# Kernel tuning notes

Hardware: AMD Instinct MI355X
Metric: run time of the kernel (lower is better)

Reference implementation:

```python
import jax, jax.numpy as jnp
import numpy as np

N, E, IN, HID, OUT, B = 50000, 800000, 128, 128, 64, 4096
EPS = 1e-5


def setup_inputs() -> dict:
    key = jax.random.key(0)
    ks = jax.random.split(key, 12)
    x = jax.random.normal(ks[0], (N, IN), jnp.float32)
    edge_index = jax.random.randint(ks[1], (2, E), 0, N, dtype=jnp.int32).astype(jnp.int64)
    target_index = jax.random.randint(ks[2], (B,), 0, N, dtype=jnp.int32).astype(jnp.int64)

    def lin(k, i, o):
        return jax.random.normal(k, (i, o), jnp.float32) * (1.0 / np.sqrt(i))

    return {
        'x': x, 'edge_index': edge_index, 'target_index': target_index,
        'W0': lin(ks[3], IN, HID), 'b0': jnp.zeros((HID,), jnp.float32),
        'W1': lin(ks[4], HID, HID), 'b1': jnp.zeros((HID,), jnp.float32),
        'W2': lin(ks[5], HID, HID), 'b2': jnp.zeros((HID,), jnp.float32),
        'g0': jnp.ones((HID,), jnp.float32), 'bt0': jnp.zeros((HID,), jnp.float32),
        'g1': jnp.ones((HID,), jnp.float32), 'bt1': jnp.zeros((HID,), jnp.float32),
        'f1w': lin(ks[6], HID, HID), 'f1b': jnp.zeros((HID,), jnp.float32),
        'f2w': lin(ks[7], HID, OUT), 'f2b': jnp.zeros((OUT,), jnp.float32),
    }


def _gcn_layer(h, W, b, src, dst, norm):
    # GCNConv: D^-1/2 (A+I) D^-1/2 (h W) + b  (self-loops already in src/dst)
    h = h @ W                                        # [N, out]
    msg = h[src] * norm[:, None]                     # [E+N, out]
    return jax.ops.segment_sum(msg, dst, num_segments=N) + b


def _batchnorm(h, g, bt):
    mu = jnp.mean(h, axis=0)
    var = jnp.mean((h - mu) ** 2, axis=0)            # biased, as torch BN
    return g * (h - mu) * jax.lax.rsqrt(var + EPS) + bt


def reference(x, edge_index, target_index, W0, b0, W1, b1, W2, b2,
              g0, bt0, g1, bt1, f1w, f1b, f2w, f2b):
    loop = jnp.arange(N, dtype=edge_index.dtype)
    src = jnp.concatenate([edge_index[0], loop])
    dst = jnp.concatenate([edge_index[1], loop])
    deg = jax.ops.segment_sum(jnp.ones_like(dst, jnp.float32), dst, num_segments=N)
    dinv = jax.lax.rsqrt(deg)                        # deg >= 1 via self-loops
    norm = dinv[src] * dinv[dst]                     # [E+N]

    h = _gcn_layer(x, W0, b0, src, dst, norm)
    h = jax.nn.relu(_batchnorm(h, g0, bt0))
    h = _gcn_layer(h, W1, b1, src, dst, norm)
    h = jax.nn.relu(_batchnorm(h, g1, bt1))
    h = _gcn_layer(h, W2, b2, src, dst, norm)

    # target_index.unsqueeze(1).expand(-1,-1) -> [B,1]; pool squeezes dim 1
    t = h[target_index]                              # [B, HID]
    t = jax.nn.relu(t @ f1w + f1b)                   # FeedForwardNetwork layer1 (dropout=0)
    return t @ f2w + f2b                             # [B, OUT]
```

## Files before the change

### kernel.cpp

```cpp
#include <hip/hip_runtime.h>


static const int GNN5566_NN  = 50000;
static const int GNN5566_NE  = 800000;
static const int GNN5566_NB  = 4096;
static const int GNN5566_CAP = 64;

static const int GNN5566_NBUCK  = (GNN5566_NN + 63) / 64;
static const int GNN5566_NCHUNK = 64;
static const int GNN5566_CHUNK  = GNN5566_NE / GNN5566_NCHUNK;

static const int GNN5566_WSLOT = 17408;

typedef short gnn5566_s16x8 __attribute__((ext_vector_type(8)));
typedef float gnn5566_f32x4 __attribute__((ext_vector_type(4)));

static __device__ inline float gnn5566_b2f(unsigned short h){
  return __uint_as_float(((unsigned int)h) << 16);
}
static __device__ inline unsigned short gnn5566_f2b(float f){
  unsigned int u = __float_as_uint(f);
  u += 0x7fffu + ((u >> 16) & 1u);
  return (unsigned short)(u >> 16);
}
static __device__ inline float gnn5566_loadf(const void* p, long long i, int isF32){
  if (isF32) return ((const float*)p)[i];
  return gnn5566_b2f(((const unsigned short*)p)[i]);
}

__global__ void GNNEncoder_5566277616090_prep(const void* W0, const void* W1,
                                              const void* W2, const void* f1w,
                                              const void* f2w, unsigned short* wT,
                                              const int* ei, const int* tgt,
                                              int* flags, int* done,
                                              unsigned int* histT){
  __shared__ unsigned short lt[128][129];
  __shared__ int h[GNN5566_NBUCK];
  __shared__ int sFlag;
  int b = blockIdx.x, tid = threadIdx.x;

  if (b == 69) {
    if (tid < 8) done[tid] = 0;
    if (tid < 64) {
      int o1 = ei[2*tid + 1];
      int o2 = tgt[2*tid + 1];
      unsigned int w = ((const unsigned int*)W0)[tid];
      unsigned int e = (w >> 7) & 255u;
      unsigned long long m1 = __ballot(o1 != 0);
      unsigned long long m2 = __ballot(o2 != 0);
      unsigned long long m3 = __ballot(e >= 96u && e <= 134u);
      if (tid == 0) {
        flags[0] = (m1 == 0ull) ? 1 : 0;
        flags[1] = (m2 == 0ull) ? 1 : 0;
        flags[2] = (__popcll(m3) >= 56) ? 0 : 1;
      }
    }
    return;
  }

  if (b >= 64) {
    if (tid < 64) {
      unsigned int w = ((const unsigned int*)W0)[tid];
      unsigned int e = (w >> 7) & 255u;
      unsigned long long m3 = __ballot(e >= 96u && e <= 134u);
      if (tid == 0) sFlag = (__popcll(m3) >= 56) ? 0 : 1;
    }
    __syncthreads();
    int f32 = sFlag;
    int slot = b - 64;
    const void* src = (slot == 0) ? W0 : (slot == 1) ? W1 : (slot == 2) ? W2
                    : (slot == 3) ? f1w : f2w;
    int wide = (slot != 4);
    int tot = wide ? 16384 : 8192;
    for (int i = tid; i < tot; i += 256) {
      int k = wide ? (i >> 7) : (i >> 6);
      int c = wide ? (i & 127) : (i & 63);
      lt[k][c] = f32 ? gnn5566_f2b(((const float*)src)[i])
                     : ((const unsigned short*)src)[i];
    }
    __syncthreads();
    unsigned short* out = wT + slot * GNN5566_WSLOT;
    int wtot = wide ? 2048 : 1024;
    for (int j = tid; j < wtot; j += 256) {
      int c = j >> 4, k8 = (j & 15) << 3;
      unsigned int p0 = (unsigned int)lt[k8    ][c] | ((unsigned int)lt[k8+1][c] << 16);
      unsigned int p1 = (unsigned int)lt[k8 + 2][c] | ((unsigned int)lt[k8+3][c] << 16);
      unsigned int p2 = (unsigned int)lt[k8 + 4][c] | ((unsigned int)lt[k8+5][c] << 16);
      unsigned int p3 = (unsigned int)lt[k8 + 6][c] | ((unsigned int)lt[k8+7][c] << 16);
      uint4 v; v.x = p0; v.y = p1; v.z = p2; v.w = p3;
      *(uint4*)(out + c * 136 + k8) = v;
    }
    return;
  }

  if (tid < 64) {
    int o1 = ei[2*tid + 1];
    unsigned long long m1 = __ballot(o1 != 0);
    if (tid == 0) sFlag = (m1 == 0ull) ? 1 : 0;
  }
  for (int i = tid; i < GNN5566_NBUCK; i += 256) h[i] = 0;
  __syncthreads();
  int f = sFlag;
  int base = b * GNN5566_CHUNK;
  for (int i = tid; i < GNN5566_CHUNK; i += 256) {
    int e = base + i;
    int d = f ? ((const int2*)ei)[GNN5566_NE + e].x : ei[GNN5566_NE + e];
    atomicAdd(&h[d >> 6], 1);
  }
  __syncthreads();
  for (int i = tid; i < GNN5566_NBUCK; i += 256)
    histT[i * GNN5566_NCHUNK + b] = (unsigned int)h[i];
}

__global__ void GNNEncoder_5566277616090_fillS1(unsigned int* histT, int* btot,
                                                int* segStart, int* doneCtr){
  __shared__ int sv[256];
  __shared__ int lastFlag;
  int tid  = threadIdx.x;
  int wv   = (int)(blockIdx.x * 4u + (tid >> 6));
  int lane = tid & 63;

  if (wv < GNN5566_NBUCK) {
    unsigned int* row = histT + wv * GNN5566_NCHUNK;
    int s = (int)row[lane];
    int incl = s;
    #pragma unroll
    for (int off = 1; off < 64; off <<= 1) {
      int t = __shfl_up(incl, off, 64);
      if (lane >= off) incl += t;
    }
    row[lane] = (unsigned int)(incl - s);
    if (lane == 63) atomicExch(&btot[wv], incl);
  }
  __syncthreads();
  if (tid == 0) {
    __threadfence();
    lastFlag = (atomicAdd(doneCtr, 1) == (int)gridDim.x - 1);
  }
  __syncthreads();
  if (!lastFlag) return;

  int i0 = tid * 4;
  int v0 = (i0     < GNN5566_NBUCK) ? atomicAdd(&btot[i0    ], 0) : 0;
  int v1 = (i0 + 1 < GNN5566_NBUCK) ? atomicAdd(&btot[i0 + 1], 0) : 0;
  int v2 = (i0 + 2 < GNN5566_NBUCK) ? atomicAdd(&btot[i0 + 2], 0) : 0;
  int v3 = (i0 + 3 < GNN5566_NBUCK) ? atomicAdd(&btot[i0 + 3], 0) : 0;
  int t01 = v0 + v1, t012 = t01 + v2, T = t012 + v3;
  sv[tid] = T;
  __syncthreads();
  for (int off = 1; off < 256; off <<= 1) {
    int add = (tid >= off) ? sv[tid - off] : 0;
    __syncthreads();
    sv[tid] += add;
    __syncthreads();
  }
  int excl = sv[tid] - T;
  if (i0     < GNN5566_NBUCK) segStart[i0]     = excl;
  if (i0 + 1 < GNN5566_NBUCK) segStart[i0 + 1] = excl + v0;
  if (i0 + 2 < GNN5566_NBUCK) segStart[i0 + 2] = excl + t01;
  if (i0 + 3 < GNN5566_NBUCK) segStart[i0 + 3] = excl + t012;
  if (tid == 0) segStart[GNN5566_NBUCK] = GNN5566_NE;
}

__global__ void GNNEncoder_5566277616090_fillScatter(const int* ei,
                                                     const unsigned int* histT,
                                                     const int* segStart,
                                                     unsigned int* sorted,
                                                     const int* flags){
  __shared__ int cur[GNN5566_NBUCK];
  int tid = threadIdx.x, chunk = blockIdx.x;
  for (int b = tid; b < GNN5566_NBUCK; b += 256)
    cur[b] = (int)histT[b * GNN5566_NCHUNK + chunk] + segStart[b];
  __syncthreads();
  int f = flags[0];
  int base = chunk * GNN5566_CHUNK;
  for (int i = tid; i < GNN5566_CHUNK; i += 256) {
    int e = base + i;
    int s = f ? ((const int2*)ei)[e].x                : ei[e];
    int d = f ? ((const int2*)ei)[GNN5566_NE + e].x   : ei[GNN5566_NE + e];
    int p = atomicAdd(&cur[d >> 6], 1);
    sorted[p] = ((unsigned int)s << 6) | (unsigned int)(d & 63);
  }
}

__global__ void GNNEncoder_5566277616090_fillB(const int* segStart,
                                               const unsigned int* sorted,
                                               unsigned short* colIdx16, int* cnt,
                                               float* dinv){
  __shared__ unsigned int lbuf[64 * 32];
  __shared__ int lcnt[64];
  int b   = blockIdx.x;
  int tid = threadIdx.x;
  if (tid < 64) lcnt[tid] = 0;
  __syncthreads();

  int s0 = segStart[b];
  int n  = segStart[b + 1] - s0;
  const unsigned int* bp = sorted + s0;
  unsigned short* lists = (unsigned short*)lbuf;
  for (int i = tid; i < n; i += 256) {
    unsigned int w = bp[i];
    int d = (int)(w & 63u);
    int s = (int)(w >> 6);
    int p = atomicAdd(&lcnt[d], 1);
    if (p < GNN5566_CAP) lists[d * 64 + p] = (unsigned short)s;
  }
  __syncthreads();

  if (tid < 64) {
    int node = b * 64 + tid;
    if (node < GNN5566_NN) {
      int c = lcnt[tid];
      cnt[node]  = c;
      dinv[node] = rsqrtf((float)(c + 1));
    }
  }
  unsigned int* out = (unsigned int*)colIdx16;
  for (int idx = tid; idx < 2048; idx += 256) {
    int d = idx >> 5;
    int node = b * 64 + d;
    if (node < GNN5566_NN)
      out[(long long)node * 32 + (idx & 31)] = lbuf[idx];
  }
}

__global__ void GNNEncoder_5566277616090_kernel(const void* A,
                                                const unsigned short* wT,
                                                unsigned short* Out, int nRows,
                                                const float* bnA, const float* bnC,
                                                const float* rowScale,
                                                const void* bias, int reluOut,
                                                int aExternal, const int* flags)
{
  __shared__ __align__(16) unsigned short gnnLw[128 * 136];
  __shared__ float lbnA[128], lbnC[128], lbias[128];
  int tid = threadIdx.x;
  int wF32 = flags[2];
  int aF32 = aExternal ? wF32 : 0;

  int wave = tid >> 6, lane = tid & 63;
  int q = lane >> 4, ln = lane & 15;
  int rowBase = blockIdx.x * 64 + wave * 16;
  int r  = rowBase + ln;
  int cr = (r < nRows) ? r : (nRows - 1);
  float rs = rowScale ? rowScale[cr] : 1.0f;
  int useBN = (bnA != 0);

  uint4  rawU[4];
  float4 rawF[8];
  if (aF32) {
    const float4* ap = (const float4*)A + (long long)cr * 32 + q * 2;
    #pragma unroll
    for (int kk = 0; kk < 4; ++kk) { rawF[2*kk] = ap[kk*8]; rawF[2*kk+1] = ap[kk*8+1]; }
  } else {
    const uint4* ap = (const uint4*)A + (long long)cr * 16 + q;
    #pragma unroll
    for (int kk = 0; kk < 4; ++kk) rawU[kk] = ap[kk * 4];
  }

  {
    const uint4* src = (const uint4*)wT;
    uint4* dst = (uint4*)gnnLw;
    for (int i = tid; i < 2176; i += 256) dst[i] = src[i];
  }
  if (tid < 128) {
    lbnA[tid]  = bnA  ? bnA[tid] : 0.0f;
    lbnC[tid]  = bnC  ? bnC[tid] : 0.0f;
    lbias[tid] = bias ? gnn5566_loadf(bias, tid, wF32) : 0.0f;
  }
  __syncthreads();

  gnn5566_s16x8 afr[4];
  #pragma unroll
  for (int kk = 0; kk < 4; ++kk) {
    int kb = kk * 32 + q * 8;
    float vals[8];
    if (aF32) {
      float4 u = rawF[2*kk], w = rawF[2*kk+1];
      vals[0] = u.x; vals[1] = u.y; vals[2] = u.z; vals[3] = u.w;
      vals[4] = w.x; vals[5] = w.y; vals[6] = w.z; vals[7] = w.w;
    } else {
      uint4 u = rawU[kk];
      vals[0] = gnn5566_b2f((unsigned short)(u.x & 0xffffu));
      vals[1] = gnn5566_b2f((unsigned short)(u.x >> 16));
      vals[2] = gnn5566_b2f((unsigned short)(u.y & 0xffffu));
      vals[3] = gnn5566_b2f((unsigned short)(u.y >> 16));
      vals[4] = gnn5566_b2f((unsigned short)(u.z & 0xffffu));
      vals[5] = gnn5566_b2f((unsigned short)(u.z >> 16));
      vals[6] = gnn5566_b2f((unsigned short)(u.w & 0xffffu));
      vals[7] = gnn5566_b2f((unsigned short)(u.w >> 16));
    }
    if (useBN) {
      float4 a0 = *(const float4*)&lbnA[kb], a1 = *(const float4*)&lbnA[kb + 4];
      float4 c0 = *(const float4*)&lbnC[kb], c1 = *(const float4*)&lbnC[kb + 4];
      vals[0] = fmaxf(vals[0] * a0.x + c0.x, 0.0f);
      vals[1] = fmaxf(vals[1] * a0.y + c0.y, 0.0f);
      vals[2] = fmaxf(vals[2] * a0.z + c0.z, 0.0f);
      vals[3] = fmaxf(vals[3] * a0.w + c0.w, 0.0f);
      vals[4] = fmaxf(vals[4] * a1.x + c1.x, 0.0f);
      vals[5] = fmaxf(vals[5] * a1.y + c1.y, 0.0f);
      vals[6] = fmaxf(vals[6] * a1.z + c1.z, 0.0f);
      vals[7] = fmaxf(vals[7] * a1.w + c1.w, 0.0f);
    }
    #pragma unroll
    for (int j = 0; j < 8; ++j) afr[kk][j] = (short)gnn5566_f2b(vals[j] * rs);
  }

  gnn5566_f32x4 zero4;
  zero4[0] = 0.0f; zero4[1] = 0.0f; zero4[2] = 0.0f; zero4[3] = 0.0f;
  gnn5566_f32x4 acc[8];
  #pragma unroll
  for (int t = 0; t < 8; ++t) acc[t] = zero4;

  #pragma unroll
  for (int kk = 0; kk < 4; ++kk) {
    int kb = kk * 32 + q * 8;
    #pragma unroll
    for (int t = 0; t < 8; ++t) {
      gnn5566_s16x8 bfr = *(const gnn5566_s16x8*)(&gnnLw[(t * 16 + ln) * 136 + kb]);
      acc[t] = __builtin_amdgcn_mfma_f32_16x16x32_bf16(afr[kk], bfr, acc[t], 0, 0, 0);
    }
  }

  __syncthreads();
  #pragma unroll
  for (int t = 0; t < 8; ++t) {
    int col = t * 16 + ln;
    float badd = lbias[col];
    #pragma unroll
    for (int rg = 0; rg < 4; ++rg) {
      float v = acc[t][rg] + badd;
      if (reluOut) v = fmaxf(v, 0.0f);
      gnnLw[(wave * 16 + q * 4 + rg) * 136 + col] = gnn5566_f2b(v);
    }
  }
  __syncthreads();
  int tRowBase = blockIdx.x * 64;
  for (int j = tid; j < 1024; j += 256) {
    int rr = j >> 4, c4 = j & 15;
    int grow = tRowBase + rr;
    if (grow < nRows) {
      uint4 v = *(const uint4*)&gnnLw[rr * 136 + c4 * 8];
      *(uint4*)&Out[(long long)grow * 128 + c4 * 8] = v;
    }
  }
}

__global__ void GNNEncoder_5566277616090_ffn(const unsigned short* A,
                                             const unsigned short* wT3,
                                             const unsigned short* wT4,
                                             void* Out, const int* tgt,
                                             const int* tgtFlag,
                                             const void* f1b, const void* fb2,
                                             const int* flags)
{
  __shared__ __align__(16) unsigned short lwA[128 * 136];
  __shared__ __align__(16) unsigned short lwB[64 * 136];
  __shared__ __align__(16) unsigned short ep[64 * 136];
  __shared__ float lb1[128];
  __shared__ float lb2[64];
  int tid = threadIdx.x;
  int f32 = flags[2];

  {
    const uint4* sA = (const uint4*)wT3;
    uint4* dA = (uint4*)lwA;
    for (int i = tid; i < 2176; i += 256) dA[i] = sA[i];
    const uint4* sB = (const uint4*)wT4;
    uint4* dB = (uint4*)lwB;
    for (int i = tid; i < 1088; i += 256) dB[i] = sB[i];
  }
  if (tid < 128) lb1[tid] = gnn5566_loadf(f1b, tid, f32);
  if (tid < 64)  lb2[tid] = gnn5566_loadf(fb2, tid, f32);
  __syncthreads();

  int wave = tid >> 6, lane = tid & 63;
  int q = lane >> 4, ln = lane & 15;
  int rowBase = blockIdx.x * 64 + wave * 16;
  int r  = rowBase + ln;
  int cr = (r < GNN5566_NB) ? r : (GNN5566_NB - 1);
  int ar = (*tgtFlag) ? tgt[2 * cr] : tgt[cr];

  gnn5566_s16x8 afr[4];
  #pragma unroll
  for (int kk = 0; kk < 4; ++kk) {
    int kb = kk * 32 + q * 8;
    const uint4* ap = (const uint4*)A + (long long)ar * 16 + (kb >> 3);
    uint4 u = ap[0];
    unsigned short e[8];
    e[0] = (unsigned short)(u.x & 0xffffu); e[1] = (unsigned short)(u.x >> 16);
    e[2] = (unsigned short)(u.y & 0xffffu); e[3] = (unsigned short)(u.y >> 16);
    e[4] = (unsigned short)(u.z & 0xffffu); e[5] = (unsigned short)(u.z >> 16);
    e[6] = (unsigned short)(u.w & 0xffffu); e[7] = (unsigned short)(u.w >> 16);
    #pragma unroll
    for (int j = 0; j < 8; ++j) afr[kk][j] = (short)e[j];
  }

  gnn5566_f32x4 zero4;
  zero4[0] = 0.0f; zero4[1] = 0.0f; zero4[2] = 0.0f; zero4[3] = 0.0f;
  gnn5566_f32x4 acc[8];
  #pragma unroll
  for (int t = 0; t < 8; ++t) acc[t] = zero4;
  #pragma unroll
  for (int kk = 0; kk < 4; ++kk) {
    int kb = kk * 32 + q * 8;
    #pragma unroll
    for (int t = 0; t < 8; ++t) {
      gnn5566_s16x8 bfr = *(const gnn5566_s16x8*)(&lwA[(t * 16 + ln) * 136 + kb]);
      acc[t] = __builtin_amdgcn_mfma_f32_16x16x32_bf16(afr[kk], bfr, acc[t], 0, 0, 0);
    }
  }
  #pragma unroll
  for (int t = 0; t < 8; ++t) {
    int col = t * 16 + ln;
    float badd = lb1[col];
    #pragma unroll
    for (int rg = 0; rg < 4; ++rg) {
      float v = fmaxf(acc[t][rg] + badd, 0.0f);
      ep[(wave * 16 + q * 4 + rg) * 136 + col] = gnn5566_f2b(v);
    }
  }
  __syncthreads();

  gnn5566_s16x8 afr2[4];
  #pragma unroll
  for (int kk = 0; kk < 4; ++kk) {
    int kb = kk * 32 + q * 8;
    afr2[kk] = *(const gnn5566_s16x8*)(&ep[(wave * 16 + ln) * 136 + kb]);
  }
  gnn5566_f32x4 acc2[4];
  #pragma unroll
  for (int t = 0; t < 4; ++t) acc2[t] = zero4;
  #pragma unroll
  for (int kk = 0; kk < 4; ++kk) {
    int kb = kk * 32 + q * 8;
    #pragma unroll
    for (int t = 0; t < 4; ++t) {
      gnn5566_s16x8 bfr = *(const gnn5566_s16x8*)(&lwB[(t * 16 + ln) * 136 + kb]);
      acc2[t] = __builtin_amdgcn_mfma_f32_16x16x32_bf16(afr2[kk], bfr, acc2[t], 0, 0, 0);
    }
  }
  #pragma unroll
  for (int t = 0; t < 4; ++t) {
    int col = t * 16 + ln;
    float badd = lb2[col];
    #pragma unroll
    for (int rg = 0; rg < 4; ++rg) {
      int grow = rowBase + q * 4 + rg;
      if (grow < GNN5566_NB) {
        float v = acc2[t][rg] + badd;
        if (f32) ((float*)Out)[(long long)grow * 64 + col] = v;
        else     ((unsigned short*)Out)[(long long)grow * 64 + col] = gnn5566_f2b(v);
      }
    }
  }
}

__global__ void GNNEncoder_5566277616090_agg(const unsigned short* hs,
                                             const unsigned short* colIdx16,
                                             const int* cnt, const float* dinv,
                                             const void* bias, unsigned short* ha,
                                             const int* flags)
{
  int gw = (int)((blockIdx.x * 256u + threadIdx.x) >> 6);
  if (gw >= GNN5566_NN) return;
  int lane = threadIdx.x & 63;
  const unsigned int* hrow = (const unsigned int*)hs;
  unsigned int sv = hrow[(long long)gw * 64 + lane];
  float a0 = __uint_as_float(sv << 16);
  float a1 = __uint_as_float(sv & 0xffff0000u);
  int m = cnt[gw]; if (m > GNN5566_CAP) m = GNN5566_CAP;
  const unsigned short* cp = colIdx16 + (long long)gw * GNN5566_CAP;
  const uint4* cp4 = (const uint4*)cp;
  int i = 0;
  for (; i + 16 <= m; i += 16) {
    uint4 iwA = cp4[i >> 3];
    uint4 iwB = cp4[(i >> 3) + 1];
    unsigned int v0  = hrow[(long long)(iwA.x & 0xffffu) * 64 + lane];
    unsigned int v1  = hrow[(long long)(iwA.x >> 16)     * 64 + lane];
    unsigned int v2  = hrow[(long long)(iwA.y & 0xffffu) * 64 + lane];
    unsigned int v3  = hrow[(long long)(iwA.y >> 16)     * 64 + lane];
    unsigned int v4  = hrow[(long long)(iwA.z & 0xffffu) * 64 + lane];
    unsigned int v5  = hrow[(long long)(iwA.z >> 16)     * 64 + lane];
    unsigned int v6  = hrow[(long long)(iwA.w & 0xffffu) * 64 + lane];
    unsigned int v7  = hrow[(long long)(iwA.w >> 16)     * 64 + lane];
    unsigned int v8  = hrow[(long long)(iwB.x & 0xffffu) * 64 + lane];
    unsigned int v9  = hrow[(long long)(iwB.x >> 16)     * 64 + lane];
    unsigned int v10 = hrow[(long long)(iwB.y & 0xffffu) * 64 + lane];
    unsigned int v11 = hrow[(long long)(iwB.y >> 16)     * 64 + lane];
    unsigned int v12 = hrow[(long long)(iwB.z & 0xffffu) * 64 + lane];
    unsigned int v13 = hrow[(long long)(iwB.z >> 16)     * 64 + lane];
    unsigned int v14 = hrow[(long long)(iwB.w & 0xffffu) * 64 + lane];
    unsigned int v15 = hrow[(long long)(iwB.w >> 16)     * 64 + lane];
    a0 += __uint_as_float(v0  << 16) + __uint_as_float(v1  << 16)
        + __uint_as_float(v2  << 16) + __uint_as_float(v3  << 16)
        + __uint_as_float(v4  << 16) + __uint_as_float(v5  << 16)
        + __uint_as_float(v6  << 16) + __uint_as_float(v7  << 16)
        + __uint_as_float(v8  << 16) + __uint_as_float(v9  << 16)
        + __uint_as_float(v10 << 16) + __uint_as_float(v11 << 16)
        + __uint_as_float(v12 << 16) + __uint_as_float(v13 << 16)
        + __uint_as_float(v14 << 16) + __uint_as_float(v15 << 16);
    a1 += __uint_as_float(v0  & 0xffff0000u) + __uint_as_float(v1  & 0xffff0000u)
        + __uint_as_float(v2  & 0xffff0000u) + __uint_as_float(v3  & 0xffff0000u)
        + __uint_as_float(v4  & 0xffff0000u) + __uint_as_float(v5  & 0xffff0000u)
        + __uint_as_float(v6  & 0xffff0000u) + __uint_as_float(v7  & 0xffff0000u)
        + __uint_as_float(v8  & 0xffff0000u) + __uint_as_float(v9  & 0xffff0000u)
        + __uint_as_float(v10 & 0xffff0000u) + __uint_as_float(v11 & 0xffff0000u)
        + __uint_as_float(v12 & 0xffff0000u) + __uint_as_float(v13 & 0xffff0000u)
        + __uint_as_float(v14 & 0xffff0000u) + __uint_as_float(v15 & 0xffff0000u);
  }
  for (; i + 8 <= m; i += 8) {
    uint4 iw = cp4[i >> 3];
    unsigned int v0 = hrow[(long long)(iw.x & 0xffffu) * 64 + lane];
    unsigned int v1 = hrow[(long long)(iw.x >> 16)     * 64 + lane];
    unsigned int v2 = hrow[(long long)(iw.y & 0xffffu) * 64 + lane];
    unsigned int v3 = hrow[(long long)(iw.y >> 16)     * 64 + lane];
    unsigned int v4 = hrow[(long long)(iw.z & 0xffffu) * 64 + lane];
    unsigned int v5 = hrow[(long long)(iw.z >> 16)     * 64 + lane];
    unsigned int v6 = hrow[(long long)(iw.w & 0xffffu) * 64 + lane];
    unsigned int v7 = hrow[(long long)(iw.w >> 16)     * 64 + lane];
    a0 += __uint_as_float(v0 << 16) + __uint_as_float(v1 << 16)
        + __uint_as_float(v2 << 16) + __uint_as_float(v3 << 16)
        + __uint_as_float(v4 << 16) + __uint_as_float(v5 << 16)
        + __uint_as_float(v6 << 16) + __uint_as_float(v7 << 16);
    a1 += __uint_as_float(v0 & 0xffff0000u) + __uint_as_float(v1 & 0xffff0000u)
        + __uint_as_float(v2 & 0xffff0000u) + __uint_as_float(v3 & 0xffff0000u)
        + __uint_as_float(v4 & 0xffff0000u) + __uint_as_float(v5 & 0xffff0000u)
        + __uint_as_float(v6 & 0xffff0000u) + __uint_as_float(v7 & 0xffff0000u);
  }
  for (; i < m; ++i) {
    unsigned int v = hrow[(long long)cp[i] * 64 + lane];
    a0 += __uint_as_float(v << 16);
    a1 += __uint_as_float(v & 0xffff0000u);
  }
  float s = dinv[gw];
  int f32 = flags[2];
  float o0 = a0 * s + gnn5566_loadf(bias, lane * 2,     f32);
  float o1 = a1 * s + gnn5566_loadf(bias, lane * 2 + 1, f32);
  unsigned int packed = (unsigned int)gnn5566_f2b(o0)
                      | (((unsigned int)gnn5566_f2b(o1)) << 16);
  ((unsigned int*)ha)[(long long)gw * 64 + lane] = packed;
}

__global__ void GNNEncoder_5566277616090_stats(const unsigned short* ha, float* partial,
                                               const void* g, const void* bt,
                                               float* bnA, float* bnC,
                                               const int* flags, int* doneCtr){
  __shared__ float red[256];
  __shared__ int lastFlag;
  const unsigned int* h32 = (const unsigned int*)ha;
  int tid = threadIdx.x;
  int cp2 = tid & 63, sub = tid >> 6;
  float s0 = 0.0f, s1 = 0.0f, q0 = 0.0f, q1 = 0.0f;
  for (int r = blockIdx.x * 4 + sub; r < GNN5566_NN; r += 512) {
    unsigned int v = h32[(long long)r * 64 + cp2];
    float a = __uint_as_float(v << 16);
    float b = __uint_as_float(v & 0xffff0000u);
    s0 += a; q0 += a * a; s1 += b; q1 += b * b;
  }
  float* prow = partial + blockIdx.x * 256;
  red[tid] = s0; __syncthreads();
  if (sub == 0) atomicExch(&prow[2*cp2],
      red[cp2] + red[64+cp2] + red[128+cp2] + red[192+cp2]);
  __syncthreads();
  red[tid] = s1; __syncthreads();
  if (sub == 0) atomicExch(&prow[2*cp2 + 1],
      red[cp2] + red[64+cp2] + red[128+cp2] + red[192+cp2]);
  __syncthreads();
  red[tid] = q0; __syncthreads();
  if (sub == 0) atomicExch(&prow[128 + 2*cp2],
      red[cp2] + red[64+cp2] + red[128+cp2] + red[192+cp2]);
  __syncthreads();
  red[tid] = q1; __syncthreads();
  if (sub == 0) atomicExch(&prow[128 + 2*cp2 + 1],
      red[cp2] + red[64+cp2] + red[128+cp2] + red[192+cp2]);
  __syncthreads();

  if (tid == 0) {
    __threadfence();
    lastFlag = (atomicAdd(doneCtr, 1) == (int)gridDim.x - 1);
  }
  __syncthreads();
  if (!lastFlag) return;

  float acc = 0.0f;
  for (int b = 0; b < (int)gridDim.x; b += 8) {
    float p0 = atomicAdd(&partial[(b    ) * 256 + tid], 0.0f);
    float p1 = atomicAdd(&partial[(b + 1) * 256 + tid], 0.0f);
    float p2 = atomicAdd(&partial[(b + 2) * 256 + tid], 0.0f);
    float p3 = atomicAdd(&partial[(b + 3) * 256 + tid], 0.0f);
    float p4 = atomicAdd(&partial[(b + 4) * 256 + tid], 0.0f);
    float p5 = atomicAdd(&partial[(b + 5) * 256 + tid], 0.0f);
    float p6 = atomicAdd(&partial[(b + 6) * 256 + tid], 0.0f);
    float p7 = atomicAdd(&partial[(b + 7) * 256 + tid], 0.0f);
    acc += ((p0 + p1) + (p2 + p3)) + ((p4 + p5) + (p6 + p7));
  }
  red[tid] = acc;
  __syncthreads();
  if (tid < 128) {
    int f32 = flags[2];
    float invN = 1.0f / (float)GNN5566_NN;
    float mu  = red[tid] * invN;
    float var = red[128 + tid] * invN - mu * mu;
    if (var < 0.0f) var = 0.0f;
    float a = gnn5566_loadf(g, tid, f32) * rsqrtf(var + 1e-5f);
    bnA[tid] = a;
    bnC[tid] = gnn5566_loadf(bt, tid, f32) - mu * a;
  }
}

extern "C" void kernel_launch(void* const* d_in, const int* in_sizes, int n_in,
                              void* d_out, int out_size, void* d_ws, size_t ws_size,
                              hipStream_t stream)
{
  const void* x   = d_in[0];
  const int*  ei  = (const int*)d_in[1];
  const int*  tgt = (const int*)d_in[2];
  const void* W0  = d_in[3];
  const void* b0  = d_in[4];
  const void* W1  = d_in[5];
  const void* b1  = d_in[6];
  const void* W2  = d_in[7];
  const void* b2  = d_in[8];
  const void* g0  = d_in[9];
  const void* bt0 = d_in[10];
  const void* g1  = d_in[11];
  const void* bt1 = d_in[12];
  const void* f1w = d_in[13];
  const void* f1b = d_in[14];
  const void* f2w = d_in[15];
  const void* fb2 = d_in[16];

  char* ws = (char*)d_ws;
  int*            segStart = (int*)           (ws + 0);
  int*            btot     = (int*)           (ws + 4096);
  int*            cnt      = (int*)           (ws + 8192);
  float*          dinv     = (float*)         (ws + 208896);
  unsigned short* wT       = (unsigned short*)(ws + 409600);
  unsigned int*   histT    = (unsigned int*)  (ws + 583936);
  unsigned int*   sorted   = (unsigned int*)  (ws + 1384960);
  unsigned short* colIdx16 = (unsigned short*)(ws + 4585216);
  unsigned short* hs       = (unsigned short*)(ws + 10985472);
  unsigned short* ha       = (unsigned short*)(ws + 23785728);
  float*          partial  = (float*)         (ws + 36585984);
  float*          bn       = (float*)         (ws + 36848128);
  int*            flags    = (int*)           (ws + 36850176);
  int*            done     = (int*)           (ws + 36850432);

  float* bn0A = bn;       float* bn0C = bn + 128;
  float* bn1A = bn + 256; float* bn1C = bn + 384;

  GNNEncoder_5566277616090_prep  <<<70, 256, 0, stream>>>(
      W0, W1, W2, f1w, f2w, wT, ei, tgt, flags, done, histT);
  GNNEncoder_5566277616090_fillS1<<<196, 256, 0, stream>>>(histT, btot, segStart, done);
  GNNEncoder_5566277616090_fillScatter<<<GNN5566_NCHUNK, 256, 0, stream>>>(
      ei, histT, segStart, sorted, flags);
  GNNEncoder_5566277616090_fillB <<<GNN5566_NBUCK, 256, 0, stream>>>(
      segStart, sorted, colIdx16, cnt, dinv);

  const int gemmGrid = (GNN5566_NN + 63) / 64;

  GNNEncoder_5566277616090_kernel<<<gemmGrid, 256, 0, stream>>>(
      x, wT, hs, GNN5566_NN, (const float*)0, (const float*)0, dinv,
      (const void*)0, 0, 1, flags);
  GNNEncoder_5566277616090_agg  <<<12500, 256, 0, stream>>>(hs, colIdx16, cnt, dinv, b0, ha, flags);
  GNNEncoder_5566277616090_stats<<<128, 256, 0, stream>>>(
      ha, partial, g0, bt0, bn0A, bn0C, flags, done + 1);

  GNNEncoder_5566277616090_kernel<<<gemmGrid, 256, 0, stream>>>(
      ha, wT + GNN5566_WSLOT, hs, GNN5566_NN, bn0A, bn0C, dinv,
      (const void*)0, 0, 0, flags);
  GNNEncoder_5566277616090_agg  <<<12500, 256, 0, stream>>>(hs, colIdx16, cnt, dinv, b1, ha, flags);
  GNNEncoder_5566277616090_stats<<<128, 256, 0, stream>>>(
      ha, partial + 32768, g1, bt1, bn1A, bn1C, flags, done + 2);

  GNNEncoder_5566277616090_kernel<<<gemmGrid, 256, 0, stream>>>(
      ha, wT + 2 * GNN5566_WSLOT, hs, GNN5566_NN, bn1A, bn1C, dinv,
      (const void*)0, 0, 0, flags);
  GNNEncoder_5566277616090_agg  <<<12500, 256, 0, stream>>>(hs, colIdx16, cnt, dinv, b2, ha, flags);

  GNNEncoder_5566277616090_ffn<<<64, 256, 0, stream>>>(
      ha, wT + 3 * GNN5566_WSLOT, wT + 4 * GNN5566_WSLOT, d_out,
      tgt, flags + 1, f1b, fb2, flags);
}
```

Measured before the change: 374.1 us.

## Merge histogram, scan and scatter into one per-chunk sort kernel

Result: faster. 356.7 us, median of 2 (-4.6%).

```diff
diff --git a/kernel.cpp b/kernel.cpp
--- a/kernel.cpp
+++ b/kernel.cpp
@@ -7,7 +7,7 @@
 static const int GNN5566_CAP = 64;
 
 static const int GNN5566_NBUCK  = (GNN5566_NN + 63) / 64;
-static const int GNN5566_NCHUNK = 64;
+static const int GNN5566_NCHUNK = 128;
 static const int GNN5566_CHUNK  = GNN5566_NE / GNN5566_NCHUNK;
 
 static const int GNN5566_WSLOT = 17408;
@@ -28,18 +28,20 @@
   return gnn5566_b2f(((const unsigned short*)p)[i]);
 }
 
-__global__ void GNNEncoder_5566277616090_prep(const void* W0, const void* W1,
-                                              const void* W2, const void* f1w,
-                                              const void* f2w, unsigned short* wT,
-                                              const int* ei, const int* tgt,
-                                              int* flags, int* done,
-                                              unsigned int* histT){
+__global__ void GNNEncoder_5566277616090_sortA(const void* W0, const void* W1,
+                                               const void* W2, const void* f1w,
+                                               const void* f2w, unsigned short* wT,
+                                               const int* ei, const int* tgt,
+                                               int* flags, int* done,
+                                               unsigned int* histC, unsigned int* prefC,
+                                               unsigned int* sorted){
   __shared__ unsigned short lt[128][129];
   __shared__ int h[GNN5566_NBUCK];
+  __shared__ int sv[256];
   __shared__ int sFlag;
   int b = blockIdx.x, tid = threadIdx.x;
 
-  if (b == 69) {
+  if (b == 133) {
     if (tid < 8) done[tid] = 0;
     if (tid < 64) {
       int o1 = ei[2*tid + 1];
@@ -58,7 +60,7 @@
     return;
   }
 
-  if (b >= 64) {
+  if (b >= 128) {
     if (tid < 64) {
       unsigned int w = ((const unsigned int*)W0)[tid];
       unsigned int e = (w >> 7) & 255u;
@@ -67,7 +69,7 @@
     }
     __syncthreads();
     int f32 = sFlag;
-    int slot = b - 64;
+    int slot = b - 128;
     const void* src = (slot == 0) ? W0 : (slot == 1) ? W1 : (slot == 2) ? W2
                     : (slot == 3) ? f1w : f2w;
     int wide = (slot != 4);
@@ -102,50 +104,19 @@
   __syncthreads();
   int f = sFlag;
   int base = b * GNN5566_CHUNK;
+
   for (int i = tid; i < GNN5566_CHUNK; i += 256) {
-    int e = base + i;
-    int d = f ? ((const int2*)ei)[GNN5566_NE + e].x : ei[GNN5566_NE + e];
+    int d = f ? ((const int2*)ei)[GNN5566_NE + base + i].x : ei[GNN5566_NE + base + i];
     atomicAdd(&h[d >> 6], 1);
   }
   __syncthreads();
-  for (int i = tid; i < GNN5566_NBUCK; i += 256)
-    histT[i * GNN5566_NCHUNK + b] = (unsigned int)h[i];
-}
-
-__global__ void GNNEncoder_5566277616090_fillS1(unsigned int* histT, int* btot,
-                                                int* segStart, int* doneCtr){
-  __shared__ int sv[256];
-  __shared__ int lastFlag;
-  int tid  = threadIdx.x;
-  int wv   = (int)(blockIdx.x * 4u + (tid >> 6));
-  int lane = tid & 63;
-
-  if (wv < GNN5566_NBUCK) {
-    unsigned int* row = histT + wv * GNN5566_NCHUNK;
-    int s = (int)row[lane];
-    int incl = s;
-    #pragma unroll
-    for (int off = 1; off < 64; off <<= 1) {
-      int t = __shfl_up(incl, off, 64);
-      if (lane >= off) incl += t;
-    }
-    row[lane] = (unsigned int)(incl - s);
-    if (lane == 63) atomicExch(&btot[wv], incl);
-  }
-  __syncthreads();
-  if (tid == 0) {
-    __threadfence();
-    lastFlag = (atomicAdd(doneCtr, 1) == (int)gridDim.x - 1);
-  }
-  __syncthreads();
-  if (!lastFlag) return;
-
-  int i0 = tid * 4;
-  int v0 = (i0     < GNN5566_NBUCK) ? atomicAdd(&btot[i0    ], 0) : 0;
-  int v1 = (i0 + 1 < GNN5566_NBUCK) ? atomicAdd(&btot[i0 + 1], 0) : 0;
-  int v2 = (i0 + 2 < GNN5566_NBUCK) ? atomicAdd(&btot[i0 + 2], 0) : 0;
-  int v3 = (i0 + 3 < GNN5566_NBUCK) ? atomicAdd(&btot[i0 + 3], 0) : 0;
-  int t01 = v0 + v1, t012 = t01 + v2, T = t012 + v3;
+
+  int b0 = tid * 4;
+  int c0 = (b0     < GNN5566_NBUCK) ? h[b0]     : 0;
+  int c1 = (b0 + 1 < GNN5566_NBUCK) ? h[b0 + 1] : 0;
+  int c2 = (b0 + 2 < GNN5566_NBUCK) ? h[b0 + 2] : 0;
+  int c3 = (b0 + 3 < GNN5566_NBUCK) ? h[b0 + 3] : 0;
+  int T = c0 + c1 + c2 + c3;
   sv[tid] = T;
   __syncthreads();
   for (int off = 1; off < 256; off <<= 1) {
@@ -155,38 +126,39 @@
     __syncthreads();
   }
   int excl = sv[tid] - T;
-  if (i0     < GNN5566_NBUCK) segStart[i0]     = excl;
-  if (i0 + 1 < GNN5566_NBUCK) segStart[i0 + 1] = excl + v0;
-  if (i0 + 2 < GNN5566_NBUCK) segStart[i0 + 2] = excl + t01;
-  if (i0 + 3 < GNN5566_NBUCK) segStart[i0 + 3] = excl + t012;
-  if (tid == 0) segStart[GNN5566_NBUCK] = GNN5566_NE;
-}
-
-__global__ void GNNEncoder_5566277616090_fillScatter(const int* ei,
-                                                     const unsigned int* histT,
-                                                     const int* segStart,
-                                                     unsigned int* sorted,
-                                                     const int* flags){
-  __shared__ int cur[GNN5566_NBUCK];
-  int tid = threadIdx.x, chunk = blockIdx.x;
-  for (int b = tid; b < GNN5566_NBUCK; b += 256)
-    cur[b] = (int)histT[b * GNN5566_NCHUNK + chunk] + segStart[b];
-  __syncthreads();
-  int f = flags[0];
-  int base = chunk * GNN5566_CHUNK;
+
+  unsigned int* hrow = histC + (long long)b * GNN5566_NBUCK;
+  unsigned int* prow = prefC + (long long)b * GNN5566_NBUCK;
+  if (b0     < GNN5566_NBUCK) { hrow[b0]     = (unsigned int)c0;
+                                prow[b0]     = (unsigned int)excl;
+                                h[b0]     = excl; }
+  if (b0 + 1 < GNN5566_NBUCK) { hrow[b0 + 1] = (unsigned int)c1;
+                                prow[b0 + 1] = (unsigned int)(excl + c0);
+                                h[b0 + 1] = excl + c0; }
+  if (b0 + 2 < GNN5566_NBUCK) { hrow[b0 + 2] = (unsigned int)c2;
+                                prow[b0 + 2] = (unsigned int)(excl + c0 + c1);
+                                h[b0 + 2] = excl + c0 + c1; }
+  if (b0 + 3 < GNN5566_NBUCK) { hrow[b0 + 3] = (unsigned int)c3;
+                                prow[b0 + 3] = (unsigned int)(excl + c0 + c1 + c2);
+                                h[b0 + 3] = excl + c0 + c1 + c2; }
+  __syncthreads();
+
   for (int i = tid; i < GNN5566_CHUNK; i += 256) {
-    int e = base + i;
-    int s = f ? ((const int2*)ei)[e].x                : ei[e];
-    int d = f ? ((const int2*)ei)[GNN5566_NE + e].x   : ei[GNN5566_NE + e];
-    int p = atomicAdd(&cur[d >> 6], 1);
-    sorted[p] = ((unsigned int)s << 6) | (unsigned int)(d & 63);
-  }
-}
-
-__global__ void GNNEncoder_5566277616090_fillB(const int* segStart,
-                                               const unsigned int* sorted,
-                                               unsigned short* colIdx16, int* cnt,
-                                               float* dinv){
+    int s, d;
+    if (f) { s = ((const int2*)ei)[base + i].x;
+             d = ((const int2*)ei)[GNN5566_NE + base + i].x; }
+    else   { s = ei[base + i];
+             d = ei[GNN5566_NE + base + i]; }
+    int p = atomicAdd(&h[d >> 6], 1);
+    sorted[base + p] = ((unsigned int)s << 6) | (unsigned int)(d & 63);
+  }
+}
+
+__global__ void GNNEncoder_5566277616090_fillB2(const unsigned int* histC,
+                                                const unsigned int* prefC,
+                                                const unsigned int* sorted,
+                                                unsigned short* colIdx16, int* cnt,
+                                                float* dinv){
   __shared__ unsigned int lbuf[64 * 32];
   __shared__ int lcnt[64];
   int b   = blockIdx.x;
@@ -194,16 +166,17 @@
   if (tid < 64) lcnt[tid] = 0;
   __syncthreads();
 
-  int s0 = segStart[b];
-  int n  = segStart[b + 1] - s0;
-  const unsigned int* bp = sorted + s0;
   unsigned short* lists = (unsigned short*)lbuf;
-  for (int i = tid; i < n; i += 256) {
-    unsigned int w = bp[i];
-    int d = (int)(w & 63u);
-    int s = (int)(w >> 6);
-    int p = atomicAdd(&lcnt[d], 1);
-    if (p < GNN5566_CAP) lists[d * 64 + p] = (unsigned short)s;
+  if (tid < GNN5566_NCHUNK) {
+    int c     = tid;
+    int len   = (int)histC[(long long)c * GNN5566_NBUCK + b];
+    int start = c * GNN5566_CHUNK + (int)prefC[(long long)c * GNN5566_NBUCK + b];
+    for (int j = 0; j < len; ++j) {
+      unsigned int w = sorted[start + j];
+      int d = (int)(w & 63u);
+      int p = atomicAdd(&lcnt[d], 1);
+      if (p < GNN5566_CAP) lists[d * 64 + p] = (unsigned short)(w >> 6);
+    }
   }
   __syncthreads();
 
@@ -632,12 +605,11 @@
   const void* fb2 = d_in[16];
 
   char* ws = (char*)d_ws;
-  int*            segStart = (int*)           (ws + 0);
-  int*            btot     = (int*)           (ws + 4096);
   int*            cnt      = (int*)           (ws + 8192);
   float*          dinv     = (float*)         (ws + 208896);
   unsigned short* wT       = (unsigned short*)(ws + 409600);
-  unsigned int*   histT    = (unsigned int*)  (ws + 583936);
+  unsigned int*   histC    = (unsigned int*)  (ws + 583936);
+  unsigned int*   prefC    = (unsigned int*)  (ws + 984320);
   unsigned int*   sorted   = (unsigned int*)  (ws + 1384960);
   unsigned short* colIdx16 = (unsigned short*)(ws + 4585216);
   unsigned short* hs       = (unsigned short*)(ws + 10985472);
@@ -650,13 +622,10 @@
   float* bn0A = bn;       float* bn0C = bn + 128;
   float* bn1A = bn + 256; float* bn1C = bn + 384;
 
-  GNNEncoder_5566277616090_prep  <<<70, 256, 0, stream>>>(
-      W0, W1, W2, f1w, f2w, wT, ei, tgt, flags, done, histT);
-  GNNEncoder_5566277616090_fillS1<<<196, 256, 0, stream>>>(histT, btot, segStart, done);
-  GNNEncoder_5566277616090_fillScatter<<<GNN5566_NCHUNK, 256, 0, stream>>>(
-      ei, histT, segStart, sorted, flags);
-  GNNEncoder_5566277616090_fillB <<<GNN5566_NBUCK, 256, 0, stream>>>(
-      segStart, sorted, colIdx16, cnt, dinv);
+  GNNEncoder_5566277616090_sortA <<<134, 256, 0, stream>>>(
+      W0, W1, W2, f1w, f2w, wT, ei, tgt, flags, done, histC, prefC, sorted);
+  GNNEncoder_5566277616090_fillB2<<<GNN5566_NBUCK, 256, 0, stream>>>(
+      histC, prefC, sorted, colIdx16, cnt, dinv);
 
   const int gemmGrid = (GNN5566_NN + 63) / 64;
 
```
